# Kernel optimization log

Measured on AMD Instinct MI355X. Metric: run time of the kernel, lower is better.

## Reference

```python
import jax, jax.numpy as jnp
import numpy as np

N_NODES = 50000
N_EDGES = 800000
D = 128


def _degrees(idx, n):
    # in/out degree via segment_sum of ones, clamped to >=1 (DGL clamp)
    ones = jnp.ones(idx.shape[0], dtype=jnp.float32)
    return jnp.clip(jax.ops.segment_sum(ones, idx, num_segments=n), 1.0)


def graph_conv(x, src, dst, W, b):
    # DGL GraphConv, norm='both', aggregate-then-matmul (in_feats == out_feats)
    n = x.shape[0]
    deg_out = _degrees(src, n)  # [N]
    deg_in = _degrees(dst, n)   # [N]
    xs = x * jax.lax.rsqrt(deg_out)[:, None]          # [N, D] pre-normalize
    msg = jax.ops.segment_sum(xs[src], dst, num_segments=n)  # gather+scatter [N, D]
    h = msg * jax.lax.rsqrt(deg_in)[:, None]
    return h @ W + b


def setup_inputs() -> dict:
    key = jax.random.key(0)
    k1, k2, k3, k4, k5 = jax.random.split(key, 5)
    x = jax.random.normal(k1, (N_NODES, D), dtype=jnp.float32)
    src = jax.random.randint(k2, (N_EDGES,), 0, N_NODES, dtype=jnp.int64)
    dst = jax.random.randint(k3, (N_EDGES,), 0, N_NODES, dtype=jnp.int64)
    scale = 1.0 / np.sqrt(D)
    W1 = jax.random.normal(k4, (D, D), dtype=jnp.float32) * scale
    W2 = jax.random.normal(k5, (D, D), dtype=jnp.float32) * scale
    b1 = jnp.zeros((D,), dtype=jnp.float32)
    b2 = jnp.zeros((D,), dtype=jnp.float32)
    return {"x": x, "src": src, "dst": dst, "W1": W1, "b1": b1, "W2": W2, "b2": b2}


def reference(x, src, dst, W1, b1, W2, b2):
    h = graph_conv(x, src, dst, W1, b1)
    h = jax.nn.relu(h)
    return graph_conv(h, src, dst, W2, b2)
```

## Files before the change

### kernel.cpp

```cpp
#include <hip/hip_runtime.h>

#define N_NODES 50000
#define N_EDGES 800000
#define D 128
#define CAP 48
#define OVF_CAP 4096

#define BINS 40
#define PNODES 1250
#define B1 64
#define CH1 ((N_EDGES + B1 - 1) / B1)
#define NW (N_NODES / 4)

typedef unsigned short bf16_t;
typedef __attribute__((ext_vector_type(8))) short short8v;
typedef __attribute__((ext_vector_type(4))) float f32x4;

__device__ inline float bf2f(bf16_t u) {
    union { unsigned int i; float f; } v;
    v.i = ((unsigned int)u) << 16;
    return v.f;
}
__device__ inline bf16_t f2bf(float f) {
    union { float f; unsigned int i; } v;
    v.f = f;
    unsigned int u = v.i;
    unsigned int r = (u + 0x7FFFu + ((u >> 16) & 1u)) >> 16;
    return (bf16_t)r;
}
__device__ inline float u2f_lo(unsigned int u) {
    union { unsigned int i; float f; } x; x.i = u << 16; return x.f;
}
__device__ inline float u2f_hi(unsigned int u) {
    union { unsigned int i; float f; } x; x.i = u & 0xFFFF0000u; return x.f;
}

__global__ __launch_bounds__(1024) void hist40_kernel(const int* __restrict__ src,
                                                      const int* __restrict__ dst,
                                                      unsigned int* __restrict__ H40,
                                                      unsigned int* __restrict__ SH, int nE) {
    __shared__ unsigned int hb[BINS];
    __shared__ unsigned int hs[NW];
    for (int i = threadIdx.x; i < NW; i += 1024) hs[i] = 0u;
    if (threadIdx.x < BINS) hb[threadIdx.x] = 0u;
    __syncthreads();
    int e0 = blockIdx.x * CH1;
    int e1 = min(e0 + CH1, nE);
    for (int e = e0 + (int)threadIdx.x; e < e1; e += 1024) {
        int s = src[e];
        int d = dst[e];
        atomicAdd(&hs[s >> 2], 1u << (8 * (s & 3)));
        atomicAdd(&hb[d / PNODES], 1u);
    }
    __syncthreads();
    if (threadIdx.x < BINS) H40[blockIdx.x * BINS + threadIdx.x] = hb[threadIdx.x];
    unsigned int* SHb = SH + (size_t)blockIdx.x * NW;
    for (int i = threadIdx.x; i < NW; i += 1024) SHb[i] = hs[i];
}

__global__ void scan40_kernel(const unsigned int* __restrict__ H40,
                              unsigned int* __restrict__ OFF40,
                              unsigned int* __restrict__ binBase,
                              unsigned int* __restrict__ binTot) {
    __shared__ unsigned int part[B1 * BINS];
    __shared__ unsigned int tot[BINS], base[BINS];
    int j = (int)threadIdx.x;
    if (j < BINS) {
        unsigned int run = 0;
        for (int b = 0; b < B1; b++) {
            part[b * BINS + j] = run;
            run += H40[b * BINS + j];
        }
        tot[j] = run;
    }
    __syncthreads();
    if (j == 0) {
        unsigned int run = 0;
        for (int q = 0; q < BINS; q++) { base[q] = run; run += tot[q]; }
    }
    __syncthreads();
    if (j < BINS) {
        binBase[j] = base[j];
        binTot[j] = tot[j];
        for (int b = 0; b < B1; b++) OFF40[b * BINS + j] = part[b * BINS + j] + base[j];
    }
}

__global__ __launch_bounds__(1024) void place40_kernel(const int* __restrict__ src,
                                                       const int* __restrict__ dst,
                                                       const unsigned int* __restrict__ OFF40,
                                                       unsigned int* __restrict__ binned, int nE) {
    __shared__ unsigned int cur[BINS];
    if (threadIdx.x < BINS) cur[threadIdx.x] = OFF40[blockIdx.x * BINS + threadIdx.x];
    __syncthreads();
    int e0 = blockIdx.x * CH1;
    int e1 = min(e0 + CH1, nE);
    for (int e = e0 + (int)threadIdx.x; e < e1; e += 1024) {
        int s = src[e];
        int d = dst[e];
        int bin = d / PNODES;
        unsigned int pos = atomicAdd(&cur[bin], 1u);
        binned[pos] = (unsigned int)(d - bin * PNODES) | ((unsigned int)s << 16);
    }
}

__global__ void sreduce_kernel(const unsigned int* __restrict__ SH, int* __restrict__ cnt_s) {
    int w = blockIdx.x * 256 + (int)threadIdx.x;
    if (w >= NW) return;
    unsigned int run = 0;
#pragma unroll 8
    for (int b = 0; b < B1; b++) run += SH[(size_t)b * NW + w];
    int4 c;
    c.x = (int)(run & 0xFFu); c.y = (int)((run >> 8) & 0xFFu);
    c.z = (int)((run >> 16) & 0xFFu); c.w = (int)(run >> 24);
    ((int4*)cnt_s)[w] = c;
}

__global__ __launch_bounds__(1024) void scatter2_kernel(
    const unsigned int* __restrict__ binned, const unsigned int* __restrict__ binBase,
    const unsigned int* __restrict__ binTot, unsigned short* __restrict__ bucket,
    int* __restrict__ cnt_d, int* __restrict__ ovf_cnt, int2* __restrict__ ovf) {
    __shared__ unsigned short bk[PNODES * CAP];
    __shared__ unsigned int cur[PNODES];
    const int j = blockIdx.x;
    const int nbeg = j * PNODES;
    for (int i = threadIdx.x; i < PNODES; i += 1024) cur[i] = 0u;
    __syncthreads();
    unsigned int b0 = binBase[j];
    unsigned int n = binTot[j];
    for (unsigned int i = threadIdx.x; i < n; i += 1024) {
        unsigned int v = binned[b0 + i];
        unsigned int dl = v & 0xFFFFu;
        unsigned int s = v >> 16;
        unsigned int q = atomicAdd(&cur[dl], 1u);
        if (q < CAP) {
            bk[dl * CAP + q] = (unsigned short)s;
        } else {
            int o = atomicAdd(ovf_cnt, 1);
            if (o < OVF_CAP) ovf[o] = make_int2(nbeg + (int)dl, (int)s);
        }
    }
    __syncthreads();
    uint4* gb = (uint4*)(bucket + (size_t)nbeg * CAP);
    const uint4* lb = (const uint4*)bk;
    const int n16 = PNODES * CAP * 2 / 16;
    for (int i = threadIdx.x; i < n16; i += 1024) gb[i] = lb[i];
    for (int i = threadIdx.x; i < PNODES; i += 1024) cnt_d[nbeg + i] = (int)cur[i];
}

__global__ void prescale_kernel(const float4* __restrict__ x, const int* __restrict__ cnt_s,
                                const int* __restrict__ cnt_d,
                                float* __restrict__ rs_out, float* __restrict__ rs_in,
                                ushort4* __restrict__ xs4, int nN) {
    int node = blockIdx.x * 8 + (threadIdx.x >> 5);
    int c = threadIdx.x & 31;
    if (node >= nN) return;
    float rs_o = 0.0f;
    if (c == 0) {
        rs_o = rsqrtf(fmaxf((float)cnt_s[node], 1.0f));
        rs_out[node] = rs_o;
        rs_in[node] = rsqrtf(fmaxf((float)cnt_d[node], 1.0f));
    }
    rs_o = __shfl(rs_o, threadIdx.x & 32);
    float4 v = x[(size_t)node * 32 + c];
    ushort4 o;
    o.x = f2bf(v.x * rs_o);
    o.y = f2bf(v.y * rs_o);
    o.z = f2bf(v.z * rs_o);
    o.w = f2bf(v.w * rs_o);
    xs4[(size_t)node * 32 + c] = o;
}

__global__ void wsplit_kernel(const float* __restrict__ W1, bf16_t* __restrict__ Wf1,
                              const float* __restrict__ W2, bf16_t* __restrict__ Wf2) {
    const float* W = blockIdx.y ? W2 : W1;
    bf16_t* Wf = blockIdx.y ? Wf2 : Wf1;
    int flat = blockIdx.x * 256 + (int)threadIdx.x;
    int lane = flat & 63;
    int c = (flat >> 6) & 7;
    int ks = flat >> 9;
    int n = c * 16 + (lane & 15);
    int kb = ks * 32 + (lane >> 4) * 8;
#pragma unroll
    for (int j = 0; j < 8; j++) {
        float w = W[(size_t)(kb + j) * D + n];
        bf16_t hi = f2bf(w);
        bf16_t lo = f2bf(w - bf2f(hi));
        Wf[(size_t)flat * 8 + j] = hi;
        Wf[(size_t)(2048 + flat) * 8 + j] = lo;
    }
}

#define LDW 132
template <bool RELU_OUTSCALE, bool OUT_BF16>
__global__ __launch_bounds__(256) void fused_layer_kernel(
    const uint4* __restrict__ xsrc,
    const int* __restrict__ cnt_d,
    const unsigned short* __restrict__ bucket,
    const int* __restrict__ ovf_cnt, const int2* __restrict__ ovf,
    const float* __restrict__ rs_in, const float* __restrict__ rs_out,
    const bf16_t* __restrict__ Wf, const float* __restrict__ bias,
    void* __restrict__ outp, int nN) {
    __shared__ float sA[64 * LDW];
    int tid = (int)threadIdx.x;
    int n0 = blockIdx.x * 64;
    int lane16 = tid & 15;
    int grp = tid >> 4;

#define ACC8(v)                                              \
    a[0] += u2f_lo(v.x); a[1] += u2f_hi(v.x);                \
    a[2] += u2f_lo(v.y); a[3] += u2f_hi(v.y);                \
    a[4] += u2f_lo(v.z); a[5] += u2f_hi(v.z);                \
    a[6] += u2f_lo(v.w); a[7] += u2f_hi(v.w);
#pragma unroll
    for (int r = 0; r < 4; r++) {
        int ln = r * 16 + grp;
        int node = n0 + ln;
        float a[8];
#pragma unroll
        for (int k = 0; k < 8; k++) a[k] = 0.f;
        if (node < nN) {
            const unsigned short* bk = bucket + (size_t)node * CAP;
            int cnt = min(cnt_d[node], CAP);
            int e = 0;
            for (; e + 3 < cnt; e += 4) {
                int s0 = bk[e], s1 = bk[e + 1], s2 = bk[e + 2], s3 = bk[e + 3];
                uint4 v0 = xsrc[(size_t)s0 * 16 + lane16];
                uint4 v1 = xsrc[(size_t)s1 * 16 + lane16];
                uint4 v2 = xsrc[(size_t)s2 * 16 + lane16];
                uint4 v3 = xsrc[(size_t)s3 * 16 + lane16];
                ACC8(v0) ACC8(v1) ACC8(v2) ACC8(v3)
            }
            for (; e < cnt; e++) {
                int s0 = bk[e];
                uint4 v0 = xsrc[(size_t)s0 * 16 + lane16];
                ACC8(v0)
            }
        }
        float* row = sA + ln * LDW + lane16 * 8;
#pragma unroll
        for (int k = 0; k < 8; k++) row[k] = a[k];
    }
#undef ACC8

    int novf = min(*ovf_cnt, OVF_CAP);
    if (novf > 0) {
        __syncthreads();
        for (int i = tid; i < novf; i += 256) {
            int2 ds = ovf[i];
            int ln = ds.x - n0;
            if ((unsigned)ln < 64u) {
                const uint4* xr = xsrc + (size_t)ds.y * 16;
                for (int c = 0; c < 16; c++) {
                    uint4 v = xr[c];
                    float* q = sA + ln * LDW + c * 8;
                    atomicAdd(q + 0, u2f_lo(v.x)); atomicAdd(q + 1, u2f_hi(v.x));
                    atomicAdd(q + 2, u2f_lo(v.y)); atomicAdd(q + 3, u2f_hi(v.y));
                    atomicAdd(q + 4, u2f_lo(v.z)); atomicAdd(q + 5, u2f_hi(v.z));
                    atomicAdd(q + 6, u2f_lo(v.w)); atomicAdd(q + 7, u2f_hi(v.w));
                }
            }
        }
    }
    __syncthreads();

    int lane = tid & 63;
    int wave = tid >> 6;
    int ar = lane & 15;
    int kg = lane >> 4;
    const float* ap = sA + (wave * 16 + ar) * LDW + kg * 8;
    short8v ahi[4], alo[4];
#pragma unroll
    for (int ks = 0; ks < 4; ks++) {
#pragma unroll
        for (int j = 0; j < 8; j++) {
            float av = ap[ks * 32 + j];
            bf16_t h = f2bf(av);
            ahi[ks][j] = (short)h;
            alo[ks][j] = (short)f2bf(av - bf2f(h));
        }
    }

    f32x4 acc[8];
#pragma unroll
    for (int c = 0; c < 8; c++) acc[c] = (f32x4){0.f, 0.f, 0.f, 0.f};

    const short8v* Bh = (const short8v*)Wf;
    const short8v* Bl = Bh + 2048;
#pragma unroll
    for (int ks = 0; ks < 4; ks++) {
#pragma unroll
        for (int c = 0; c < 8; c++) {
            int off = (ks * 8 + c) * 64 + lane;
            short8v wh = Bh[off];
            short8v wl = Bl[off];
            acc[c] = __builtin_amdgcn_mfma_f32_16x16x32_bf16(ahi[ks], wh, acc[c], 0, 0, 0);
            acc[c] = __builtin_amdgcn_mfma_f32_16x16x32_bf16(alo[ks], wh, acc[c], 0, 0, 0);
            acc[c] = __builtin_amdgcn_mfma_f32_16x16x32_bf16(ahi[ks], wl, acc[c], 0, 0, 0);
        }
    }

    int ocol = lane & 15;
#pragma unroll
    for (int r = 0; r < 4; r++) {
        int node = n0 + wave * 16 + kg * 4 + r;
        if (node >= nN) continue;
        float ri = rs_in[node];
        float ro = RELU_OUTSCALE ? rs_out[node] : 1.0f;
#pragma unroll
        for (int c = 0; c < 8; c++) {
            float v = acc[c][r] * ri + bias[c * 16 + ocol];
            if (RELU_OUTSCALE) v = fmaxf(v, 0.0f) * ro;
            if (OUT_BF16) {
                ((bf16_t*)outp)[(size_t)node * D + c * 16 + ocol] = f2bf(v);
            } else {
                ((float*)outp)[(size_t)node * D + c * 16 + ocol] = v;
            }
        }
    }
}
#undef LDW

static inline size_t align16(size_t x) { return (x + 15) & ~(size_t)15; }

extern "C" void kernel_launch(void* const* d_in, const int* in_sizes, int n_in,
                              void* d_out, int out_size, void* d_ws, size_t ws_size,
                              hipStream_t stream) {
    const float* x   = (const float*)d_in[0];
    const int*   src = (const int*)d_in[1];
    const int*   dst = (const int*)d_in[2];
    const float* W1  = (const float*)d_in[3];
    const float* b1  = (const float*)d_in[4];
    const float* W2  = (const float*)d_in[5];
    const float* b2  = (const float*)d_in[6];
    float* out = (float*)d_out;

    char* p = (char*)d_ws;
    int*            cnt_s   = (int*)p;            p += align16(N_NODES * sizeof(int));
    int*            cnt_d   = (int*)p;            p += align16(N_NODES * sizeof(int));
    int*            ovf_cnt = (int*)p;            p += align16(16 * sizeof(int));
    int2*           ovf     = (int2*)p;           p += align16((size_t)OVF_CAP * sizeof(int2));
    unsigned short* bucket  = (unsigned short*)p; p += align16((size_t)N_NODES * CAP * sizeof(unsigned short));
    float*          rs_out  = (float*)p;          p += align16(N_NODES * sizeof(float));
    float*          rs_in   = (float*)p;          p += align16(N_NODES * sizeof(float));
    bf16_t*         Wf1     = (bf16_t*)p;         p += align16((size_t)2 * 2048 * 8 * sizeof(bf16_t));
    bf16_t*         Wf2     = (bf16_t*)p;         p += align16((size_t)2 * 2048 * 8 * sizeof(bf16_t));
    unsigned int*   H40     = (unsigned int*)p;   p += align16((size_t)B1 * BINS * sizeof(unsigned int));
    unsigned int*   OFF40   = (unsigned int*)p;   p += align16((size_t)B1 * BINS * sizeof(unsigned int));
    unsigned int*   binBase = (unsigned int*)p;   p += align16(BINS * sizeof(unsigned int));
    unsigned int*   binTot  = (unsigned int*)p;   p += align16(BINS * sizeof(unsigned int));
    unsigned int*   binned  = (unsigned int*)p;   p += align16((size_t)N_EDGES * sizeof(unsigned int));
    unsigned int*   SH      = (unsigned int*)p;   p += align16((size_t)B1 * NW * sizeof(unsigned int));
    bf16_t*         xs      = (bf16_t*)p;         p += align16((size_t)N_NODES * D * sizeof(bf16_t));
    bf16_t*         hs      = (bf16_t*)p;

    hipMemsetAsync(ovf_cnt, 0, 16 * sizeof(int), stream);

    wsplit_kernel<<<dim3(8, 2), 256, 0, stream>>>(W1, Wf1, W2, Wf2);

    hist40_kernel<<<B1, 1024, 0, stream>>>(src, dst, H40, SH, N_EDGES);
    scan40_kernel<<<1, 64, 0, stream>>>(H40, OFF40, binBase, binTot);
    place40_kernel<<<B1, 1024, 0, stream>>>(src, dst, OFF40, binned, N_EDGES);
    sreduce_kernel<<<(NW + 255) / 256, 256, 0, stream>>>(SH, cnt_s);
    scatter2_kernel<<<BINS, 1024, 0, stream>>>(binned, binBase, binTot, bucket,
                                               cnt_d, ovf_cnt, ovf);

    prescale_kernel<<<(N_NODES + 7) / 8, 256, 0, stream>>>((const float4*)x, cnt_s, cnt_d,
                                                           rs_out, rs_in, (ushort4*)xs, N_NODES);

    int fgrid = (N_NODES + 63) / 64;

    fused_layer_kernel<true, true><<<fgrid, 256, 0, stream>>>(
        (const uint4*)xs, cnt_d, bucket, ovf_cnt, ovf, rs_in, rs_out, Wf1, b1, hs, N_NODES);

    fused_layer_kernel<false, false><<<fgrid, 256, 0, stream>>>(
        (const uint4*)hs, cnt_d, bucket, ovf_cnt, ovf, rs_in, rs_out, Wf2, b2, out, N_NODES);
}
```

Before: 207.3 us.

## Fold sreduce and memset into preprocessing kernels; use 512-thread fused layer blocks

```diff
diff --git a/kernel.cpp b/kernel.cpp
--- a/kernel.cpp
+++ b/kernel.cpp
@@ -11,6 +11,7 @@
 #define B1 64
 #define CH1 ((N_EDGES + B1 - 1) / B1)
 #define NW (N_NODES / 4)
+#define WPB ((NW + B1 - 1) / B1)
 
 typedef unsigned short bf16_t;
 typedef __attribute__((ext_vector_type(8))) short short8v;
@@ -38,9 +39,11 @@
 __global__ __launch_bounds__(1024) void hist40_kernel(const int* __restrict__ src,
                                                       const int* __restrict__ dst,
                                                       unsigned int* __restrict__ H40,
-                                                      unsigned int* __restrict__ SH, int nE) {
+                                                      unsigned int* __restrict__ SH,
+                                                      int* __restrict__ ovf_cnt, int nE) {
     __shared__ unsigned int hb[BINS];
     __shared__ unsigned int hs[NW];
+    if (blockIdx.x == 0 && threadIdx.x == 0) ovf_cnt[0] = 0;
     for (int i = threadIdx.x; i < NW; i += 1024) hs[i] = 0u;
     if (threadIdx.x < BINS) hb[threadIdx.x] = 0u;
     __syncthreads();
@@ -89,7 +92,9 @@
 __global__ __launch_bounds__(1024) void place40_kernel(const int* __restrict__ src,
                                                        const int* __restrict__ dst,
                                                        const unsigned int* __restrict__ OFF40,
-                                                       unsigned int* __restrict__ binned, int nE) {
+                                                       unsigned int* __restrict__ binned,
+                                                       const unsigned int* __restrict__ SH,
+                                                       int* __restrict__ cnt_s, int nE) {
     __shared__ unsigned int cur[BINS];
     if (threadIdx.x < BINS) cur[threadIdx.x] = OFF40[blockIdx.x * BINS + threadIdx.x];
     __syncthreads();
@@ -102,18 +107,16 @@
         unsigned int pos = atomicAdd(&cur[bin], 1u);
         binned[pos] = (unsigned int)(d - bin * PNODES) | ((unsigned int)s << 16);
     }
-}
-
-__global__ void sreduce_kernel(const unsigned int* __restrict__ SH, int* __restrict__ cnt_s) {
-    int w = blockIdx.x * 256 + (int)threadIdx.x;
-    if (w >= NW) return;
-    unsigned int run = 0;
+    int w = blockIdx.x * WPB + (int)threadIdx.x;
+    if ((int)threadIdx.x < WPB && w < NW) {
+        unsigned int run = 0;
 #pragma unroll 8
-    for (int b = 0; b < B1; b++) run += SH[(size_t)b * NW + w];
-    int4 c;
-    c.x = (int)(run & 0xFFu); c.y = (int)((run >> 8) & 0xFFu);
-    c.z = (int)((run >> 16) & 0xFFu); c.w = (int)(run >> 24);
-    ((int4*)cnt_s)[w] = c;
+        for (int b = 0; b < B1; b++) run += SH[(size_t)b * NW + w];
+        int4 c;
+        c.x = (int)(run & 0xFFu); c.y = (int)((run >> 8) & 0xFFu);
+        c.z = (int)((run >> 16) & 0xFFu); c.w = (int)(run >> 24);
+        ((int4*)cnt_s)[w] = c;
+    }
 }
 
 __global__ __launch_bounds__(1024) void scatter2_kernel(
@@ -193,7 +196,7 @@
 
 #define LDW 132
 template <bool RELU_OUTSCALE, bool OUT_BF16>
-__global__ __launch_bounds__(256) void fused_layer_kernel(
+__global__ __launch_bounds__(512) void fused_layer_kernel(
     const uint4* __restrict__ xsrc,
     const int* __restrict__ cnt_d,
     const unsigned short* __restrict__ bucket,
@@ -213,8 +216,8 @@
     a[4] += u2f_lo(v.z); a[5] += u2f_hi(v.z);                \
     a[6] += u2f_lo(v.w); a[7] += u2f_hi(v.w);
 #pragma unroll
-    for (int r = 0; r < 4; r++) {
-        int ln = r * 16 + grp;
+    for (int r = 0; r < 2; r++) {
+        int ln = r * 32 + grp;
         int node = n0 + ln;
         float a[8];
 #pragma unroll
@@ -246,7 +249,7 @@
     int novf = min(*ovf_cnt, OVF_CAP);
     if (novf > 0) {
         __syncthreads();
-        for (int i = tid; i < novf; i += 256) {
+        for (int i = tid; i < novf; i += 512) {
             int2 ds = ovf[i];
             int ln = ds.x - n0;
             if ((unsigned)ln < 64u) {
@@ -266,9 +269,11 @@
 
     int lane = tid & 63;
     int wave = tid >> 6;
+    int tile = wave >> 1;
+    int half = wave & 1;
     int ar = lane & 15;
     int kg = lane >> 4;
-    const float* ap = sA + (wave * 16 + ar) * LDW + kg * 8;
+    const float* ap = sA + (tile * 16 + ar) * LDW + kg * 8;
     short8v ahi[4], alo[4];
 #pragma unroll
     for (int ks = 0; ks < 4; ks++) {
@@ -281,17 +286,17 @@
         }
     }
 
-    f32x4 acc[8];
-#pragma unroll
-    for (int c = 0; c < 8; c++) acc[c] = (f32x4){0.f, 0.f, 0.f, 0.f};
+    f32x4 acc[4];
+#pragma unroll
+    for (int c = 0; c < 4; c++) acc[c] = (f32x4){0.f, 0.f, 0.f, 0.f};
 
     const short8v* Bh = (const short8v*)Wf;
     const short8v* Bl = Bh + 2048;
 #pragma unroll
     for (int ks = 0; ks < 4; ks++) {
 #pragma unroll
-        for (int c = 0; c < 8; c++) {
-            int off = (ks * 8 + c) * 64 + lane;
+        for (int c = 0; c < 4; c++) {
+            int off = (ks * 8 + half * 4 + c) * 64 + lane;
             short8v wh = Bh[off];
             short8v wl = Bl[off];
             acc[c] = __builtin_amdgcn_mfma_f32_16x16x32_bf16(ahi[ks], wh, acc[c], 0, 0, 0);
@@ -303,18 +308,19 @@
     int ocol = lane & 15;
 #pragma unroll
     for (int r = 0; r < 4; r++) {
-        int node = n0 + wave * 16 + kg * 4 + r;
+        int node = n0 + tile * 16 + kg * 4 + r;
         if (node >= nN) continue;
         float ri = rs_in[node];
         float ro = RELU_OUTSCALE ? rs_out[node] : 1.0f;
 #pragma unroll
-        for (int c = 0; c < 8; c++) {
-            float v = acc[c][r] * ri + bias[c * 16 + ocol];
+        for (int c = 0; c < 4; c++) {
+            int col = half * 64 + c * 16 + ocol;
+            float v = acc[c][r] * ri + bias[col];
             if (RELU_OUTSCALE) v = fmaxf(v, 0.0f) * ro;
             if (OUT_BF16) {
-                ((bf16_t*)outp)[(size_t)node * D + c * 16 + ocol] = f2bf(v);
+                ((bf16_t*)outp)[(size_t)node * D + col] = f2bf(v);
             } else {
-                ((float*)outp)[(size_t)node * D + c * 16 + ocol] = v;
+                ((float*)outp)[(size_t)node * D + col] = v;
             }
         }
     }
@@ -354,14 +360,11 @@
     bf16_t*         xs      = (bf16_t*)p;         p += align16((size_t)N_NODES * D * sizeof(bf16_t));
     bf16_t*         hs      = (bf16_t*)p;
 
-    hipMemsetAsync(ovf_cnt, 0, 16 * sizeof(int), stream);
-
     wsplit_kernel<<<dim3(8, 2), 256, 0, stream>>>(W1, Wf1, W2, Wf2);
 
-    hist40_kernel<<<B1, 1024, 0, stream>>>(src, dst, H40, SH, N_EDGES);
+    hist40_kernel<<<B1, 1024, 0, stream>>>(src, dst, H40, SH, ovf_cnt, N_EDGES);
     scan40_kernel<<<1, 64, 0, stream>>>(H40, OFF40, binBase, binTot);
-    place40_kernel<<<B1, 1024, 0, stream>>>(src, dst, OFF40, binned, N_EDGES);
-    sreduce_kernel<<<(NW + 255) / 256, 256, 0, stream>>>(SH, cnt_s);
+    place40_kernel<<<B1, 1024, 0, stream>>>(src, dst, OFF40, binned, SH, cnt_s, N_EDGES);
     scatter2_kernel<<<BINS, 1024, 0, stream>>>(binned, binBase, binTot, bucket,
                                                cnt_d, ovf_cnt, ovf);
 
@@ -370,9 +373,9 @@
 
     int fgrid = (N_NODES + 63) / 64;
 
-    fused_layer_kernel<true, true><<<fgrid, 256, 0, stream>>>(
+    fused_layer_kernel<true, true><<<fgrid, 512, 0, stream>>>(
         (const uint4*)xs, cnt_d, bucket, ovf_cnt, ovf, rs_in, rs_out, Wf1, b1, hs, N_NODES);
 
-    fused_layer_kernel<false, false><<<fgrid, 256, 0, stream>>>(
+    fused_layer_kernel<false, false><<<fgrid, 512, 0, stream>>>(
         (const uint4*)hs, cnt_d, bucket, ovf_cnt, ovf, rs_in, rs_out, Wf2, b2, out, N_NODES);
 }
```

Result: faster. 197.1 us (median of 2 runs) (-4.9%).
